# Performance work log

Hardware: AMD Instinct MI355X
Metric: run time of the kernel (lower is better)

The kernel has to match this reference:

```python
import jax, jax.numpy as jnp
import numpy as np

N_NODES = 50000
D = 128            # input_dim == hidden_dim == output_dim
N_EDGES = 800000   # 2 relation types concatenated
BN_EPS = 1e-5


def _gcn_conv(x, W, b, src, dst, n):
    # PyG GCNConv: add self loops, symmetric normalization, gather-scatter aggregate.
    h = x @ W                                   # [N, D]
    loop = jnp.arange(n)
    s = jnp.concatenate([src, loop])
    d = jnp.concatenate([dst, loop])
    deg = jax.ops.segment_sum(jnp.ones_like(s, dtype=h.dtype), d, num_segments=n)
    dinv = jnp.where(deg > 0, jax.lax.rsqrt(deg), 0.0)
    norm = dinv[s] * dinv[d]                    # [E+N]
    agg = jax.ops.segment_sum(h[s] * norm[:, None], d, num_segments=n)  # [N, D]
    return agg + b


def _batch_norm(x, gamma, beta):
    # BatchNorm1d training-mode math (biased variance over node axis)
    m = x.mean(axis=0)
    v = x.var(axis=0)
    return (x - m) * jax.lax.rsqrt(v + BN_EPS) * gamma + beta


def _gcn_layer(x, src, dst, W, b, gamma, beta, n):
    h = _gcn_conv(x, W, b, src, dst, n)
    h = jax.nn.relu(_batch_norm(h, gamma, beta))
    return h + x  # residual (in_features == out_features); dropout = identity (eval)


def setup_inputs() -> dict:
    key = jax.random.key(0)
    ks = jax.random.split(key, 8)
    x = jax.random.normal(ks[0], (N_NODES, D), dtype=jnp.float32)
    edge_index = jax.random.randint(ks[1], (2, N_EDGES), 0, N_NODES, dtype=jnp.int64)
    sc = 1.0 / np.sqrt(D)
    return {
        "x": x,
        "edge_index": edge_index,
        "W1": jax.random.normal(ks[2], (D, D), dtype=jnp.float32) * sc,
        "b1": jnp.zeros((D,), dtype=jnp.float32),
        "g1": jnp.ones((D,), dtype=jnp.float32),
        "be1": jnp.zeros((D,), dtype=jnp.float32),
        "W2": jax.random.normal(ks[3], (D, D), dtype=jnp.float32) * sc,
        "b2": jnp.zeros((D,), dtype=jnp.float32),
        "g2": jnp.ones((D,), dtype=jnp.float32),
        "be2": jnp.zeros((D,), dtype=jnp.float32),
        "Wa": jax.random.normal(ks[4], (D, 1), dtype=jnp.float32) * sc,
        "ba": jnp.zeros((1,), dtype=jnp.float32),
    }


def reference(x, edge_index, W1, b1, g1, be1, W2, b2, g2, be2, Wa, ba):
    n = x.shape[0]
    src, dst = edge_index[0], edge_index[1]
    h = _gcn_layer(x, src, dst, W1, b1, g1, be1, n)
    h = _gcn_layer(h, src, dst, W2, b2, g2, be2, n)
    att = jax.nn.softmax(jnp.tanh(h @ Wa + ba), axis=0)  # softmax over nodes
    return h * att
```

## Files before the change

### kernel.cpp

```cpp
#include <hip/hip_runtime.h>
#include <hip/hip_fp16.h>

#define NN 50000
#define DD 128
#define NE 800000
#define BN_EPS 1e-5f
#define NBUCK 196
#define TILE_A 4096

typedef _Float16 f16x8 __attribute__((ext_vector_type(8)));
typedef float f32x4 __attribute__((ext_vector_type(4)));

__global__ void k_hist(const int* __restrict__ dst, int* __restrict__ cnt, int ne) {
    int i = blockIdx.x * blockDim.x + threadIdx.x;
    if (i < ne) atomicAdd(&cnt[dst[i]], 1);
}

__global__ __launch_bounds__(256) void k_bsum(const int* __restrict__ cnt,
                                              int* __restrict__ bsum, int n) {
    __shared__ int red[256];
    int i = blockIdx.x * 256 + threadIdx.x;
    int v = (i < n) ? cnt[i] : 0;
    red[threadIdx.x] = v;
    __syncthreads();
    for (int off = 128; off > 0; off >>= 1) {
        if (threadIdx.x < off) red[threadIdx.x] += red[threadIdx.x + off];
        __syncthreads();
    }
    if (threadIdx.x == 0) bsum[blockIdx.x] = red[0];
}

__global__ __launch_bounds__(256) void k_bscan(int* __restrict__ bsum, int nb) {
    __shared__ int sh[256];
    int t = threadIdx.x;
    sh[t] = (t < nb) ? bsum[t] : 0;
    __syncthreads();
    for (int off = 1; off < 256; off <<= 1) {
        int add = (t >= off) ? sh[t - off] : 0;
        __syncthreads();
        sh[t] += add;
        __syncthreads();
    }
    if (t < nb) bsum[t] = sh[t];
}

__global__ __launch_bounds__(256) void k_rowp(const int* __restrict__ cnt,
                                              const int* __restrict__ bsum,
                                              int* __restrict__ rowp,
                                              int* __restrict__ cursor,
                                              int* __restrict__ bucketCur,
                                              float* __restrict__ dinv,
                                              float* __restrict__ sumsZ, int n) {
    if (blockIdx.x == 0) {
        for (int i = threadIdx.x; i < 8256; i += 256) sumsZ[i] = 0.f;
    }
    __shared__ int sh[256];
    int t = threadIdx.x;
    int i = blockIdx.x * 256 + t;
    int v = (i < n) ? cnt[i] : 0;
    sh[t] = v;
    __syncthreads();
    for (int off = 1; off < 256; off <<= 1) {
        int add = (t >= off) ? sh[t - off] : 0;
        __syncthreads();
        sh[t] += add;
        __syncthreads();
    }
    int base = (blockIdx.x > 0) ? bsum[blockIdx.x - 1] : 0;
    int excl = base + sh[t] - v;
    if (i < n) {
        rowp[i] = excl;
        cursor[i] = excl;
        dinv[i] = 1.0f / sqrtf((float)(v + 1));
        if ((i & 255) == 0) bucketCur[i >> 8] = excl;
        if (i == n - 1) rowp[n] = excl + v;
    }
}

__global__ __launch_bounds__(256) void k_binA(const int* __restrict__ src,
                                              const int* __restrict__ dst,
                                              int* __restrict__ bucketCur,
                                              unsigned* __restrict__ evS, int ne) {
    __shared__ int hcnt[NBUCK];
    __shared__ int hbase[NBUCK];
    int tid = threadIdx.x;
    for (int i = tid; i < NBUCK; i += 256) hcnt[i] = 0;
    __syncthreads();
    int base = blockIdx.x * TILE_A;
    int lim = ne - base;
    if (lim > TILE_A) lim = TILE_A;
    for (int i = tid; i < lim; i += 256) {
        int d = dst[base + i];
        atomicAdd(&hcnt[d >> 8], 1);
    }
    __syncthreads();
    for (int b = tid; b < NBUCK; b += 256) {
        hbase[b] = atomicAdd(&bucketCur[b], hcnt[b]);
        hcnt[b] = 0;
    }
    __syncthreads();
    for (int i = tid; i < lim; i += 256) {
        int d = dst[base + i];
        int s = src[base + i];
        int bk = d >> 8;
        int rank = atomicAdd(&hcnt[bk], 1);
        evS[hbase[bk] + rank] = (unsigned)s | ((unsigned)(d & 255) << 16);
    }
}

__global__ __launch_bounds__(256) void k_binB(const unsigned* __restrict__ evS,
                                              const int* __restrict__ rowp,
                                              int* __restrict__ cursor,
                                              unsigned* __restrict__ ev, int n) {
    int b = blockIdx.x;
    int node0 = b << 8;
    int lo = rowp[node0];
    int nhi = node0 + 256;
    if (nhi > n) nhi = n;
    int hi = rowp[nhi];
    for (int p = lo + (int)threadIdx.x; p < hi; p += 256) {
        unsigned r = evS[p];
        int node = node0 + (int)(r >> 16);
        int pos = atomicAdd(&cursor[node], 1);
        ev[pos] = r & 0xFFFFu;
    }
}

__global__ __launch_bounds__(256) void k_wprep(const float* __restrict__ W1,
                                               const float* __restrict__ W2,
                                               __half* __restrict__ Wf) {
    int widx = blockIdx.x & 1;
    const float* W = widx ? W2 : W1;
    __half* outp = Wf + (size_t)widx * DD * DD;
    int s = (blockIdx.x >> 1) * 256 + threadIdx.x;
    int l = s & 63;
    int ks = (s >> 6) & 3;
    int cb = s >> 8;
    int col = cb * 16 + (l & 15);
    int kbase = ks * 32 + (l >> 4) * 8;
    __align__(16) __half tmp[8];
    #pragma unroll
    for (int j = 0; j < 8; j++) tmp[j] = __float2half_rn(W[(kbase + j) * DD + col]);
    *(uint4*)(outp + s * 8) = *(uint4*)tmp;
}

#define GTILE 64
__global__ __launch_bounds__(256) void k_gemm(const float* __restrict__ A,
                                              const float* __restrict__ res,
                                              const float* __restrict__ sums,
                                              const float* __restrict__ gamma,
                                              const float* __restrict__ beta,
                                              float* __restrict__ Hout,
                                              const float* __restrict__ dscale,
                                              const __half* __restrict__ Wf,
                                              __half* __restrict__ C, int n) {
    __shared__ __half sW[DD * DD];
    __shared__ __half sA[GTILE * DD];
    __shared__ float s_scale[DD], s_shift[DD];
    int tid = threadIdx.x;
    int wave = tid >> 6;
    int lane = tid & 63;
    bool fused = (res != nullptr);

    {
        const float4* wg = (const float4*)Wf;
        float4* ws = (float4*)sW;
        for (int i = tid; i < DD * DD / 8; i += 256) ws[i] = wg[i];
    }
    if (fused && tid < DD) {
        float ssum = 0.f, qsum = 0.f;
        #pragma unroll
        for (int b = 0; b < 16; b++) {
            ssum += sums[b * 256 + tid];
            qsum += sums[b * 256 + 128 + tid];
        }
        float inv_n = 1.0f / (float)n;
        float mean = ssum * inv_n;
        float var = qsum * inv_n - mean * mean;
        float sc = gamma[tid] * (1.0f / sqrtf(var + BN_EPS));
        s_scale[tid] = sc;
        s_shift[tid] = beta[tid] - mean * sc;
    }

    int ntiles = (n + GTILE - 1) / GTILE;
    for (int t = blockIdx.x; t < ntiles; t += gridDim.x) {
        int row0 = t * GTILE;
        __syncthreads();
        {
            const float4* Av = (const float4*)(A + (size_t)row0 * DD);
            const float4* Rv = (const float4*)(res + (size_t)row0 * DD);
            float4* Hv = (float4*)(Hout + (size_t)row0 * DD);
            for (int i = tid; i < GTILE * DD / 4; i += 256) {
                int r = i >> 5;
                int kq = i & 31;
                bool rowok = (row0 + r < n);
                float4 v = make_float4(0.f, 0.f, 0.f, 0.f);
                if (rowok) v = Av[i];
                if (fused) {
                    float4 rv = make_float4(0.f, 0.f, 0.f, 0.f);
                    if (rowok) rv = Rv[i];
                    int f4 = kq * 4;
                    v.x = fmaxf(v.x * s_scale[f4]     + s_shift[f4],     0.f) + rv.x;
                    v.y = fmaxf(v.y * s_scale[f4 + 1] + s_shift[f4 + 1], 0.f) + rv.y;
                    v.z = fmaxf(v.z * s_scale[f4 + 2] + s_shift[f4 + 2], 0.f) + rv.z;
                    v.w = fmaxf(v.w * s_scale[f4 + 3] + s_shift[f4 + 3], 0.f) + rv.w;
                    if (rowok) Hv[i] = v;
                }
                __half2 p0 = __floats2half2_rn(v.x, v.y);
                __half2 p1 = __floats2half2_rn(v.z, v.w);
                uint2 pk;
                pk.x = *(unsigned*)&p0;
                pk.y = *(unsigned*)&p1;
                int slot = ((r >> 4) * 4 + (kq >> 3)) * 64 +
                           (((kq >> 1) & 3) << 4) + (r & 15);
                int byte = slot * 16 + (kq & 1) * 8;
                byte ^= ((byte >> 9) & 7) << 4;
                *(uint2*)((char*)sA + byte) = pk;
            }
        }
        __syncthreads();

        f32x4 acc[8];
        #pragma unroll
        for (int cb = 0; cb < 8; cb++) acc[cb] = (f32x4)(0.0f);
        f16x8 af[4];
        #pragma unroll
        for (int ks = 0; ks < 4; ks++) {
            int rb = ((wave * 4 + ks) * 64 + lane) * 16;
            rb ^= ((rb >> 9) & 7) << 4;
            af[ks] = *(const f16x8*)((const char*)sA + rb);
        }
        #pragma unroll
        for (int cb = 0; cb < 8; cb++) {
            #pragma unroll
            for (int ks = 0; ks < 4; ks++) {
                f16x8 bf = *(const f16x8*)(sW + ((cb * 4 + ks) * 64 + lane) * 8);
                acc[cb] = __builtin_amdgcn_mfma_f32_16x16x32_f16(af[ks], bf,
                                                                 acc[cb], 0, 0, 0);
            }
        }

        float dv[4];
        #pragma unroll
        for (int rr = 0; rr < 4; rr++) {
            int row = row0 + wave * 16 + (lane >> 4) * 4 + rr;
            dv[rr] = (row < n) ? dscale[row] : 1.f;
        }

        __half* sC = sA + wave * (16 * DD);
        #pragma unroll
        for (int cb = 0; cb < 8; cb++) {
            int col = cb * 16 + (lane & 15);
            #pragma unroll
            for (int rr = 0; rr < 4; rr++) {
                int grow = (lane >> 4) * 4 + rr;
                sC[grow * DD + (col ^ ((grow & 3) << 4))] =
                    __float2half(acc[cb][rr] * dv[rr]);
            }
        }
        __syncthreads();
        #pragma unroll
        for (int i2 = 0; i2 < 4; i2++) {
            int o = (i2 * 64 + lane) * 8;
            int grow = o >> 7;
            int col0 = o & 127;
            int row = row0 + wave * 16 + grow;
            if (row < n) {
                uint4 val = *(uint4*)(sC + grow * DD + (col0 ^ ((grow & 3) << 4)));
                *(uint4*)(C + (size_t)row * DD + col0) = val;
            }
        }
    }
}

#define ACC8(raw) { const __half2* hp_ = (const __half2*)&(raw);               \
    float2 c0_ = __half22float2(hp_[0]); float2 c1_ = __half22float2(hp_[1]);  \
    float2 c2_ = __half22float2(hp_[2]); float2 c3_ = __half22float2(hp_[3]);  \
    a[0] += c0_.x; a[1] += c0_.y; a[2] += c1_.x; a[3] += c1_.y;                \
    a[4] += c2_.x; a[5] += c2_.y; a[6] += c3_.x; a[7] += c3_.y; }

__global__ __launch_bounds__(256) void k_agg(const __half* __restrict__ h,
                                             const int* __restrict__ rowp,
                                             const unsigned* __restrict__ ev,
                                             const float* __restrict__ dinv,
                                             const float* __restrict__ bias,
                                             float* __restrict__ out,
                                             float* __restrict__ sums, int n) {
    int tid = threadIdx.x;
    int grp = tid >> 4;
    int m = tid & 15;
    int node = blockIdx.x * 16 + grp;
    bool activ = node < n;

    int beg = 0, end = 0;
    float di = 0.f;
    if (activ) { beg = rowp[node]; end = rowp[node + 1]; di = dinv[node]; }

    float sf[8] = {0.f, 0.f, 0.f, 0.f, 0.f, 0.f, 0.f, 0.f};
    float bf[8];
    {
        float4 b0 = *(const float4*)(bias + m * 8);
        float4 b1 = *(const float4*)(bias + m * 8 + 4);
        bf[0] = b0.x; bf[1] = b0.y; bf[2] = b0.z; bf[3] = b0.w;
        bf[4] = b1.x; bf[5] = b1.y; bf[6] = b1.z; bf[7] = b1.w;
        if (activ) {
            float4 raw = *(const float4*)(h + (size_t)node * DD + m * 8);
            const __half2* hp = (const __half2*)&raw;
            float2 s0 = __half22float2(hp[0]);
            float2 s1 = __half22float2(hp[1]);
            float2 s2 = __half22float2(hp[2]);
            float2 s3 = __half22float2(hp[3]);
            sf[0] = s0.x; sf[1] = s0.y; sf[2] = s1.x; sf[3] = s1.y;
            sf[4] = s2.x; sf[5] = s2.y; sf[6] = s3.x; sf[7] = s3.y;
        }
    }

    float a[8] = {0.f, 0.f, 0.f, 0.f, 0.f, 0.f, 0.f, 0.f};
    int e = beg;
    int cnt4 = (end - beg) >> 2;
    if (cnt4 > 0) {
        unsigned s0 = ev[e], s1 = ev[e + 1], s2 = ev[e + 2], s3 = ev[e + 3];
        float4 r0 = *(const float4*)(h + (size_t)s0 * DD + m * 8);
        float4 r1 = *(const float4*)(h + (size_t)s1 * DD + m * 8);
        float4 r2 = *(const float4*)(h + (size_t)s2 * DD + m * 8);
        float4 r3 = *(const float4*)(h + (size_t)s3 * DD + m * 8);
        for (int g = 1; g < cnt4; g++) {
            e += 4;
            unsigned t0 = ev[e], t1 = ev[e + 1], t2 = ev[e + 2], t3 = ev[e + 3];
            float4 q0 = *(const float4*)(h + (size_t)t0 * DD + m * 8);
            float4 q1 = *(const float4*)(h + (size_t)t1 * DD + m * 8);
            float4 q2 = *(const float4*)(h + (size_t)t2 * DD + m * 8);
            float4 q3 = *(const float4*)(h + (size_t)t3 * DD + m * 8);
            ACC8(r0); ACC8(r1); ACC8(r2); ACC8(r3);
            r0 = q0; r1 = q1; r2 = q2; r3 = q3;
        }
        ACC8(r0); ACC8(r1); ACC8(r2); ACC8(r3);
        e += 4;
    }
    for (; e < end; e++) {
        unsigned s = ev[e];
        float4 raw = *(const float4*)(h + (size_t)s * DD + m * 8);
        ACC8(raw);
    }

    float o[8];
    #pragma unroll
    for (int j = 0; j < 8; j++) o[j] = di * (a[j] + sf[j]) + bf[j];
    if (activ) {
        float* op = out + (size_t)node * DD + m * 8;
        *(float4*)op = make_float4(o[0], o[1], o[2], o[3]);
        *(float4*)(op + 4) = make_float4(o[4], o[5], o[6], o[7]);
    }

    __shared__ float rs[16][132];
    #pragma unroll
    for (int j = 0; j < 8; j++) rs[grp][m * 8 + j] = activ ? o[j] : 0.f;
    __syncthreads();

    int bank = blockIdx.x & 15;
    if (tid < 128) {
        float s = 0.f;
        #pragma unroll
        for (int r2 = 0; r2 < 16; r2++) s += rs[r2][tid];
        atomicAdd(&sums[bank * 256 + tid], s);
    } else {
        int f = tid - 128;
        float q = 0.f;
        #pragma unroll
        for (int r2 = 0; r2 < 16; r2++) { float v = rs[r2][f]; q += v * v; }
        atomicAdd(&sums[bank * 256 + 128 + f], q);
    }
}

__global__ __launch_bounds__(256) void k_bn(const float* __restrict__ X,
                                            const float* __restrict__ res,
                                            const float* __restrict__ sums,
                                            const float* __restrict__ gamma,
                                            const float* __restrict__ beta,
                                            const float* __restrict__ Wa,
                                            const float* __restrict__ ba,
                                            float* __restrict__ out,
                                            float* __restrict__ evec,
                                            float* __restrict__ Zb, int n) {
    __shared__ float s_scale[128], s_shift[128];
    if (threadIdx.x < 128) {
        int ff = threadIdx.x;
        float ssum = 0.f, qsum = 0.f;
        #pragma unroll
        for (int b = 0; b < 16; b++) {
            ssum += sums[b * 256 + ff];
            qsum += sums[b * 256 + 128 + ff];
        }
        float inv_n = 1.0f / (float)n;
        float mean = ssum * inv_n;
        float var = qsum * inv_n - mean * mean;
        float sc = gamma[ff] * (1.0f / sqrtf(var + BN_EPS));
        s_scale[ff] = sc;
        s_shift[ff] = beta[ff] - mean * sc;
    }
    __syncthreads();
    int idx = blockIdx.x * 256 + threadIdx.x;
    int total = n * (DD / 4);
    int f = (threadIdx.x & 31) * 4;
    float o[4] = {0.f, 0.f, 0.f, 0.f};
    if (idx < total) {
        float4 v = ((const float4*)X)[idx];
        float4 rv = ((const float4*)res)[idx];
        float vi[4] = {v.x, v.y, v.z, v.w};
        float ri[4] = {rv.x, rv.y, rv.z, rv.w};
        #pragma unroll
        for (int j = 0; j < 4; j++) {
            float x = vi[j] * s_scale[f + j] + s_shift[f + j];
            x = fmaxf(x, 0.f);
            o[j] = x + ri[j];
        }
        ((float4*)out)[idx] = make_float4(o[0], o[1], o[2], o[3]);
    }
    if (Wa != nullptr) {
        float t = 0.f;
        if (idx < total) {
            float4 wv = *(const float4*)(Wa + f);
            t = o[0] * wv.x + o[1] * wv.y + o[2] * wv.z + o[3] * wv.w;
        }
        #pragma unroll
        for (int m = 16; m >= 1; m >>= 1) t += __shfl_xor(t, m);
        __shared__ float part[8];
        if ((threadIdx.x & 31) == 0) {
            float ev = 0.f;
            if (idx < total) {
                ev = expf(tanhf(t + ba[0]));
                evec[idx >> 5] = ev;
            }
            part[threadIdx.x >> 5] = ev;
        }
        __syncthreads();
        if (threadIdx.x == 0) {
            float z = part[0] + part[1] + part[2] + part[3] +
                      part[4] + part[5] + part[6] + part[7];
            atomicAdd(&Zb[blockIdx.x & 63], z);
        }
    }
}

__global__ __launch_bounds__(256) void k_out(const float* __restrict__ H,
                                             const float* __restrict__ evec,
                                             const float* __restrict__ Zb,
                                             float* __restrict__ out, int n) {
    __shared__ float sZ;
    if (threadIdx.x == 0) {
        float z = 0.f;
        #pragma unroll
        for (int i = 0; i < 64; i++) z += Zb[i];
        sZ = z;
    }
    __syncthreads();
    int idx = blockIdx.x * blockDim.x + threadIdx.x;
    int total = n * (DD / 4);
    if (idx >= total) return;
    int node = idx >> 5;
    float s = evec[node] / sZ;
    float4 h = ((const float4*)H)[idx];
    ((float4*)out)[idx] = make_float4(h.x * s, h.y * s, h.z * s, h.w * s);
}

extern "C" void kernel_launch(void* const* d_in, const int* in_sizes, int n_in,
                              void* d_out, int out_size, void* d_ws, size_t ws_size,
                              hipStream_t stream) {
    const float* x   = (const float*)d_in[0];
    const int* eidx  = (const int*)d_in[1];
    const float* W1  = (const float*)d_in[2];
    const float* b1  = (const float*)d_in[3];
    const float* g1  = (const float*)d_in[4];
    const float* be1 = (const float*)d_in[5];
    const float* W2  = (const float*)d_in[6];
    const float* b2  = (const float*)d_in[7];
    const float* g2  = (const float*)d_in[8];
    const float* be2 = (const float*)d_in[9];
    const float* Wa  = (const float*)d_in[10];
    const float* ba  = (const float*)d_in[11];
    float* out = (float*)d_out;

    const int* srcp = eidx;
    const int* dstp = eidx + NE;

    float* bufA = (float*)d_ws;
    float* bufB = bufA + (size_t)NN * DD;
    float* bufC = bufB + (size_t)NN * DD;
    unsigned* ev = (unsigned*)(bufC + (size_t)NN * DD);
    float* dinv = (float*)(ev + NE);
    float* evec = dinv + NN;
    float* sums = evec + NN;
    float* Zb   = sums + 8192;
    int* cnt    = (int*)(Zb + 64);
    int* rowp   = cnt + NN;
    int* cursor = rowp + NN + 64;
    int* bsum   = cursor + NN;
    int* bucketCur = bsum + 256;
    __half* Wf  = (__half*)(bucketCur + 256);

    __half* hH  = (__half*)bufA;
    unsigned* evS = (unsigned*)bufB;

    float* sumsL1 = sums;
    float* sumsL2 = sums + 4096;

    const int nscan = (NN + 255) / 256;

    k_wprep<<<16, 256, 0, stream>>>(W1, W2, Wf);

    hipMemsetAsync(cnt, 0, (size_t)NN * sizeof(int), stream);
    k_hist<<<(NE + 255) / 256, 256, 0, stream>>>(dstp, cnt, NE);
    k_bsum<<<nscan, 256, 0, stream>>>(cnt, bsum, NN);
    k_bscan<<<1, 256, 0, stream>>>(bsum, nscan);
    k_rowp<<<nscan, 256, 0, stream>>>(cnt, bsum, rowp, cursor, bucketCur, dinv,
                                      sums, NN);
    k_binA<<<(NE + TILE_A - 1) / TILE_A, 256, 0, stream>>>(srcp, dstp,
                                                           bucketCur, evS, NE);
    k_binB<<<NBUCK, 256, 0, stream>>>(evS, rowp, cursor, ev, NN);

    int gemm_grid = (NN + GTILE - 1) / GTILE;
    int agg_grid  = (NN + 15) / 16;
    int ew_grid   = (NN * (DD / 4) + 255) / 256;

    k_gemm<<<gemm_grid, 256, 0, stream>>>(x, nullptr, nullptr, nullptr, nullptr,
                                          nullptr, dinv, Wf, hH, NN);
    k_agg<<<agg_grid, 256, 0, stream>>>(hH, rowp, ev, dinv, b1, bufB, sumsL1, NN);

    k_gemm<<<gemm_grid, 256, 0, stream>>>(bufB, x, sumsL1, g1, be1, bufC,
                                          dinv, Wf + (size_t)DD * DD, hH, NN);
    k_agg<<<agg_grid, 256, 0, stream>>>(hH, rowp, ev, dinv, b2, bufB, sumsL2, NN);
    k_bn<<<ew_grid, 256, 0, stream>>>(bufB, bufC, sumsL2, g2, be2, Wa, ba,
                                      bufC, evec, Zb, NN);

    k_out<<<ew_grid, 256, 0, stream>>>(bufC, evec, Zb, out, NN);
}
```

Before: 315.9 us.

## Build CSR via bucket counts only and fold weight prep into GEMM

Replaces the per-node histogram plus three-kernel scan with a two-pass bucket count (binA1/binA2) and computes per-node counts, row pointers and dinv inside binB with a local shared-memory histogram and scan. This removes the global per-node atomics, the memset of the node count array and several launches. Weight conversion to the swizzled fp16 layout is moved into each GEMM block, which removes the k_wprep launch but makes every block reconvert W from fp32 with strided loads. An extra barrier is added in the GEMM before the output staging, presumably to guard reuse of sA.

```diff
diff --git a/kernel.cpp b/kernel.cpp
--- a/kernel.cpp
+++ b/kernel.cpp
@@ -11,91 +11,51 @@
 typedef _Float16 f16x8 __attribute__((ext_vector_type(8)));
 typedef float f32x4 __attribute__((ext_vector_type(4)));
 
-__global__ void k_hist(const int* __restrict__ dst, int* __restrict__ cnt, int ne) {
-    int i = blockIdx.x * blockDim.x + threadIdx.x;
-    if (i < ne) atomicAdd(&cnt[dst[i]], 1);
-}
-
-__global__ __launch_bounds__(256) void k_bsum(const int* __restrict__ cnt,
-                                              int* __restrict__ bsum, int n) {
-    __shared__ int red[256];
-    int i = blockIdx.x * 256 + threadIdx.x;
-    int v = (i < n) ? cnt[i] : 0;
-    red[threadIdx.x] = v;
-    __syncthreads();
-    for (int off = 128; off > 0; off >>= 1) {
-        if (threadIdx.x < off) red[threadIdx.x] += red[threadIdx.x + off];
-        __syncthreads();
-    }
-    if (threadIdx.x == 0) bsum[blockIdx.x] = red[0];
-}
-
-__global__ __launch_bounds__(256) void k_bscan(int* __restrict__ bsum, int nb) {
-    __shared__ int sh[256];
-    int t = threadIdx.x;
-    sh[t] = (t < nb) ? bsum[t] : 0;
-    __syncthreads();
-    for (int off = 1; off < 256; off <<= 1) {
-        int add = (t >= off) ? sh[t - off] : 0;
-        __syncthreads();
-        sh[t] += add;
-        __syncthreads();
-    }
-    if (t < nb) bsum[t] = sh[t];
-}
-
-__global__ __launch_bounds__(256) void k_rowp(const int* __restrict__ cnt,
-                                              const int* __restrict__ bsum,
-                                              int* __restrict__ rowp,
-                                              int* __restrict__ cursor,
-                                              int* __restrict__ bucketCur,
-                                              float* __restrict__ dinv,
-                                              float* __restrict__ sumsZ, int n) {
-    if (blockIdx.x == 0) {
-        for (int i = threadIdx.x; i < 8256; i += 256) sumsZ[i] = 0.f;
-    }
-    __shared__ int sh[256];
-    int t = threadIdx.x;
-    int i = blockIdx.x * 256 + t;
-    int v = (i < n) ? cnt[i] : 0;
-    sh[t] = v;
-    __syncthreads();
-    for (int off = 1; off < 256; off <<= 1) {
-        int add = (t >= off) ? sh[t - off] : 0;
-        __syncthreads();
-        sh[t] += add;
-        __syncthreads();
-    }
-    int base = (blockIdx.x > 0) ? bsum[blockIdx.x - 1] : 0;
-    int excl = base + sh[t] - v;
-    if (i < n) {
-        rowp[i] = excl;
-        cursor[i] = excl;
-        dinv[i] = 1.0f / sqrtf((float)(v + 1));
-        if ((i & 255) == 0) bucketCur[i >> 8] = excl;
-        if (i == n - 1) rowp[n] = excl + v;
-    }
-}
-
-__global__ __launch_bounds__(256) void k_binA(const int* __restrict__ src,
-                                              const int* __restrict__ dst,
-                                              int* __restrict__ bucketCur,
-                                              unsigned* __restrict__ evS, int ne) {
+__global__ __launch_bounds__(256) void k_binA1(const int* __restrict__ dst,
+                                               int* __restrict__ bucketCnt, int ne) {
+    __shared__ int hcnt[NBUCK];
+    int tid = threadIdx.x;
+    for (int i = tid; i < NBUCK; i += 256) hcnt[i] = 0;
+    __syncthreads();
+    int base = blockIdx.x * TILE_A;
+    int lim = ne - base;
+    if (lim > TILE_A) lim = TILE_A;
+    for (int i = tid; i < lim; i += 256) atomicAdd(&hcnt[dst[base + i] >> 8], 1);
+    __syncthreads();
+    for (int b = tid; b < NBUCK; b += 256)
+        if (hcnt[b]) atomicAdd(&bucketCnt[b], hcnt[b]);
+}
+
+__global__ __launch_bounds__(256) void k_binA2(const int* __restrict__ src,
+                                               const int* __restrict__ dst,
+                                               const int* __restrict__ bucketCnt,
+                                               int* __restrict__ bucketRes,
+                                               unsigned* __restrict__ evS, int ne) {
+    __shared__ int sc[256];
+    __shared__ int sExcl[256];
     __shared__ int hcnt[NBUCK];
     __shared__ int hbase[NBUCK];
     int tid = threadIdx.x;
+    int v = (tid < NBUCK) ? bucketCnt[tid] : 0;
+    sc[tid] = v;
+    __syncthreads();
+    for (int off = 1; off < 256; off <<= 1) {
+        int add = (tid >= off) ? sc[tid - off] : 0;
+        __syncthreads();
+        sc[tid] += add;
+        __syncthreads();
+    }
+    sExcl[tid] = sc[tid] - v;
     for (int i = tid; i < NBUCK; i += 256) hcnt[i] = 0;
     __syncthreads();
+
     int base = blockIdx.x * TILE_A;
     int lim = ne - base;
     if (lim > TILE_A) lim = TILE_A;
-    for (int i = tid; i < lim; i += 256) {
-        int d = dst[base + i];
-        atomicAdd(&hcnt[d >> 8], 1);
-    }
+    for (int i = tid; i < lim; i += 256) atomicAdd(&hcnt[dst[base + i] >> 8], 1);
     __syncthreads();
     for (int b = tid; b < NBUCK; b += 256) {
-        hbase[b] = atomicAdd(&bucketCur[b], hcnt[b]);
+        hbase[b] = hcnt[b] ? (sExcl[b] + atomicAdd(&bucketRes[b], hcnt[b])) : 0;
         hcnt[b] = 0;
     }
     __syncthreads();
@@ -109,39 +69,59 @@
 }
 
 __global__ __launch_bounds__(256) void k_binB(const unsigned* __restrict__ evS,
-                                              const int* __restrict__ rowp,
-                                              int* __restrict__ cursor,
-                                              unsigned* __restrict__ ev, int n) {
+                                              const int* __restrict__ bucketCnt,
+                                              unsigned* __restrict__ ev,
+                                              int* __restrict__ rowp,
+                                              float* __restrict__ dinv, int n) {
+    __shared__ int sc[256];
+    __shared__ int ncnt[256];
+    __shared__ int nbase[256];
+    __shared__ int ncur[256];
+    int tid = threadIdx.x;
     int b = blockIdx.x;
+
+    int v = (tid < NBUCK) ? bucketCnt[tid] : 0;
+    sc[tid] = v;
+    __syncthreads();
+    for (int off = 1; off < 256; off <<= 1) {
+        int add = (tid >= off) ? sc[tid - off] : 0;
+        __syncthreads();
+        sc[tid] += add;
+        __syncthreads();
+    }
+    int lo = sc[b] - ((b < NBUCK) ? bucketCnt[b] : 0);
+    int cnt_b = bucketCnt[b];
+
+    ncnt[tid] = 0;
+    __syncthreads();
+    for (int p = tid; p < cnt_b; p += 256)
+        atomicAdd(&ncnt[evS[lo + p] >> 16], 1);
+    __syncthreads();
+    int nv = ncnt[tid];
+    sc[tid] = nv;
+    __syncthreads();
+    for (int off = 1; off < 256; off <<= 1) {
+        int add = (tid >= off) ? sc[tid - off] : 0;
+        __syncthreads();
+        sc[tid] += add;
+        __syncthreads();
+    }
+    nbase[tid] = sc[tid] - nv;
+    ncur[tid] = sc[tid] - nv;
     int node0 = b << 8;
-    int lo = rowp[node0];
-    int nhi = node0 + 256;
-    if (nhi > n) nhi = n;
-    int hi = rowp[nhi];
-    for (int p = lo + (int)threadIdx.x; p < hi; p += 256) {
-        unsigned r = evS[p];
-        int node = node0 + (int)(r >> 16);
-        int pos = atomicAdd(&cursor[node], 1);
-        ev[pos] = r & 0xFFFFu;
-    }
-}
-
-__global__ __launch_bounds__(256) void k_wprep(const float* __restrict__ W1,
-                                               const float* __restrict__ W2,
-                                               __half* __restrict__ Wf) {
-    int widx = blockIdx.x & 1;
-    const float* W = widx ? W2 : W1;
-    __half* outp = Wf + (size_t)widx * DD * DD;
-    int s = (blockIdx.x >> 1) * 256 + threadIdx.x;
-    int l = s & 63;
-    int ks = (s >> 6) & 3;
-    int cb = s >> 8;
-    int col = cb * 16 + (l & 15);
-    int kbase = ks * 32 + (l >> 4) * 8;
-    __align__(16) __half tmp[8];
-    #pragma unroll
-    for (int j = 0; j < 8; j++) tmp[j] = __float2half_rn(W[(kbase + j) * DD + col]);
-    *(uint4*)(outp + s * 8) = *(uint4*)tmp;
+    int node = node0 + tid;
+    if (node < n) {
+        rowp[node] = lo + nbase[tid];
+        dinv[node] = 1.0f / sqrtf((float)(nv + 1));
+    }
+    if (b == NBUCK - 1 && tid == 0) rowp[n] = lo + cnt_b;
+    __syncthreads();
+    for (int p = tid; p < cnt_b; p += 256) {
+        unsigned r = evS[lo + p];
+        int ln = r >> 16;
+        int rank = atomicAdd(&ncur[ln], 1);
+        ev[lo + rank] = r & 0xFFFFu;
+    }
 }
 
 #define GTILE 64
@@ -152,7 +132,7 @@
                                               const float* __restrict__ beta,
                                               float* __restrict__ Hout,
                                               const float* __restrict__ dscale,
-                                              const __half* __restrict__ Wf,
+                                              const float* __restrict__ W,
                                               __half* __restrict__ C, int n) {
     __shared__ __half sW[DD * DD];
     __shared__ __half sA[GTILE * DD];
@@ -163,9 +143,18 @@
     bool fused = (res != nullptr);
 
     {
-        const float4* wg = (const float4*)Wf;
-        float4* ws = (float4*)sW;
-        for (int i = tid; i < DD * DD / 8; i += 256) ws[i] = wg[i];
+        for (int s = tid; s < DD * DD / 8; s += 256) {
+            int l = s & 63;
+            int ks = (s >> 6) & 3;
+            int cb = s >> 8;
+            int col = cb * 16 + (l & 15);
+            int kbase = ks * 32 + (l >> 4) * 8;
+            __align__(16) __half tmp[8];
+            #pragma unroll
+            for (int j = 0; j < 8; j++)
+                tmp[j] = __float2half_rn(W[(kbase + j) * DD + col]);
+            *(uint4*)(sW + s * 8) = *(uint4*)tmp;
+        }
     }
     if (fused && tid < DD) {
         float ssum = 0.f, qsum = 0.f;
@@ -240,6 +229,8 @@
             }
         }
 
+        __syncthreads();
+
         float dv[4];
         #pragma unroll
         for (int rr = 0; rr < 4; rr++) {
@@ -489,14 +480,11 @@
     unsigned* ev = (unsigned*)(bufC + (size_t)NN * DD);
     float* dinv = (float*)(ev + NE);
     float* evec = dinv + NN;
-    float* sums = evec + NN;
+    int* bucketCnt = (int*)(evec + NN);
+    int* bucketRes = bucketCnt + 256;
+    float* sums = (float*)(bucketRes + 256);
     float* Zb   = sums + 8192;
-    int* cnt    = (int*)(Zb + 64);
-    int* rowp   = cnt + NN;
-    int* cursor = rowp + NN + 64;
-    int* bsum   = cursor + NN;
-    int* bucketCur = bsum + 256;
-    __half* Wf  = (__half*)(bucketCur + 256);
+    int* rowp   = (int*)(Zb + 64);
 
     __half* hH  = (__half*)bufA;
     unsigned* evS = (unsigned*)bufB;
@@ -504,30 +492,23 @@
     float* sumsL1 = sums;
     float* sumsL2 = sums + 4096;
 
-    const int nscan = (NN + 255) / 256;
-
-    k_wprep<<<16, 256, 0, stream>>>(W1, W2, Wf);
-
-    hipMemsetAsync(cnt, 0, (size_t)NN * sizeof(int), stream);
-    k_hist<<<(NE + 255) / 256, 256, 0, stream>>>(dstp, cnt, NE);
-    k_bsum<<<nscan, 256, 0, stream>>>(cnt, bsum, NN);
-    k_bscan<<<1, 256, 0, stream>>>(bsum, nscan);
-    k_rowp<<<nscan, 256, 0, stream>>>(cnt, bsum, rowp, cursor, bucketCur, dinv,
-                                      sums, NN);
-    k_binA<<<(NE + TILE_A - 1) / TILE_A, 256, 0, stream>>>(srcp, dstp,
-                                                           bucketCur, evS, NE);
-    k_binB<<<NBUCK, 256, 0, stream>>>(evS, rowp, cursor, ev, NN);
+    hipMemsetAsync(bucketCnt, 0, (size_t)(256 + 256 + 8192 + 64) * sizeof(int),
+                   stream);
+    const int nA = (NE + TILE_A - 1) / TILE_A;
+    k_binA1<<<nA, 256, 0, stream>>>(dstp, bucketCnt, NE);
+    k_binA2<<<nA, 256, 0, stream>>>(srcp, dstp, bucketCnt, bucketRes, evS, NE);
+    k_binB<<<NBUCK, 256, 0, stream>>>(evS, bucketCnt, ev, rowp, dinv, NN);
 
     int gemm_grid = (NN + GTILE - 1) / GTILE;
     int agg_grid  = (NN + 15) / 16;
     int ew_grid   = (NN * (DD / 4) + 255) / 256;
 
     k_gemm<<<gemm_grid, 256, 0, stream>>>(x, nullptr, nullptr, nullptr, nullptr,
-                                          nullptr, dinv, Wf, hH, NN);
+                                          nullptr, dinv, W1, hH, NN);
     k_agg<<<agg_grid, 256, 0, stream>>>(hH, rowp, ev, dinv, b1, bufB, sumsL1, NN);
 
     k_gemm<<<gemm_grid, 256, 0, stream>>>(bufB, x, sumsL1, g1, be1, bufC,
-                                          dinv, Wf + (size_t)DD * DD, hH, NN);
+                                          dinv, W2, hH, NN);
     k_agg<<<agg_grid, 256, 0, stream>>>(hH, rowp, ev, dinv, b2, bufB, sumsL2, NN);
     k_bn<<<ew_grid, 256, 0, stream>>>(bufB, bufC, sumsL2, g2, be2, Wa, ba,
                                       bufC, evec, Zb, NN);
```

New measurement: 273.3 us. -13.5%, faster.
